# Kernel tuning notes

Measured on AMD Instinct MI355X. Metric: run time of the kernel, lower is better.

Reference implementation:

```python
import jax, jax.numpy as jnp
import numpy as np

D = 1024
H = 16
HD = D // H

def setup_inputs() -> dict:
    key = jax.random.key(0)
    ks = jax.random.split(key, 5)
    scale = 1.0 / np.sqrt(D)
    x = jax.random.normal(ks[0], (2, 2048, D), dtype=jnp.float32)
    W_qkv = jax.random.uniform(ks[1], (D, 3 * D), minval=-scale, maxval=scale, dtype=jnp.float32)
    b_qkv = jax.random.uniform(ks[2], (3 * D,), minval=-scale, maxval=scale, dtype=jnp.float32)
    W_out = jax.random.uniform(ks[3], (D, D), minval=-scale, maxval=scale, dtype=jnp.float32)
    b_out = jax.random.uniform(ks[4], (D,), minval=-scale, maxval=scale, dtype=jnp.float32)
    return {"x": x, "W_qkv": W_qkv, "b_qkv": b_qkv, "W_out": W_out, "b_out": b_out}

def reference(x, W_qkv, b_qkv, W_out, b_out):
    B, S, _ = x.shape
    qkv = x @ W_qkv + b_qkv  # [B,S,3D]
    qkv = qkv.reshape(B, S, 3, H, HD).transpose(2, 0, 3, 1, 4)  # [3,B,H,S,HD]
    q, k, v = qkv[0], qkv[1], qkv[2]
    scores = jnp.einsum('bhsd,bhtd->bhst', q, k) / jnp.sqrt(jnp.float32(HD))
    probs = jax.nn.softmax(scores, axis=-1)
    attn = jnp.einsum('bhst,bhtd->bhsd', probs, v)  # [B,H,S,HD]
    attn = attn.transpose(0, 2, 1, 3).reshape(B, S, D)
    return attn @ W_out + b_out
```

## Files before the change

### kernel.cpp

```cpp
#include <hip/hip_runtime.h>


typedef short bf16x8 __attribute__((ext_vector_type(8)));
typedef float f32x4 __attribute__((ext_vector_type(4)));

__device__ __forceinline__ unsigned short f2bf(float f) {
  unsigned u = __float_as_uint(f);
  u = (u + 0x7fffu + ((u >> 16) & 1u)) >> 16;
  return (unsigned short)u;
}
__device__ __forceinline__ unsigned pack_bf2(float lo, float hi) {
  unsigned a = __float_as_uint(lo) + 0x8000u;
  unsigned b = __float_as_uint(hi) + 0x8000u;
  return __builtin_amdgcn_perm(b, a, 0x07060302);
}
__device__ __forceinline__ void load_lds16(const unsigned short* g, unsigned short* l) {
  __builtin_amdgcn_global_load_lds(
      (const __attribute__((address_space(1))) void*)g,
      (__attribute__((address_space(3))) void*)l, 16, 0, 0);
}

__global__ __launch_bounds__(256) void cvt_f32_bf16(
    const float* __restrict__ in, unsigned short* __restrict__ out, int n)
{
  const int i = (blockIdx.x * 256 + threadIdx.x) * 8;
  if (i >= n) return;
  float4 f0 = *(const float4*)(in + i);
  float4 f1 = *(const float4*)(in + i + 4);
  union { unsigned short u[8]; uint4 v; } pk;
  pk.u[0] = f2bf(f0.x); pk.u[1] = f2bf(f0.y); pk.u[2] = f2bf(f0.z); pk.u[3] = f2bf(f0.w);
  pk.u[4] = f2bf(f1.x); pk.u[5] = f2bf(f1.y); pk.u[6] = f2bf(f1.z); pk.u[7] = f2bf(f1.w);
  *(uint4*)(out + i) = pk.v;
}

__global__ __launch_bounds__(256) void transpose_cvt(
    const float* __restrict__ in, unsigned short* __restrict__ out, int R, int C)
{
  __shared__ float tile[64][65];
  const int tid = threadIdx.x;
  const int r0 = blockIdx.y * 64, c0 = blockIdx.x * 64;
  {
    const int rr = tid >> 4;
    const int cc = (tid & 15) * 4;
#pragma unroll
    for (int it = 0; it < 4; ++it) {
      float4 f = *(const float4*)&in[(size_t)(r0 + rr + 16 * it) * C + c0 + cc];
      tile[rr + 16 * it][cc + 0] = f.x;
      tile[rr + 16 * it][cc + 1] = f.y;
      tile[rr + 16 * it][cc + 2] = f.z;
      tile[rr + 16 * it][cc + 3] = f.w;
    }
  }
  __syncthreads();
  {
    const int cr = tid >> 2;
    const int rk = (tid & 3) * 16;
    union { unsigned short u[16]; uint4 v[2]; } pk;
#pragma unroll
    for (int j = 0; j < 16; ++j) pk.u[j] = f2bf(tile[rk + j][cr]);
    uint4* dst = (uint4*)&out[(size_t)(c0 + cr) * R + r0 + rk];
    dst[0] = pk.v[0];
    dst[1] = pk.v[1];
  }
}

template <int MODE>
__global__ __launch_bounds__(256) void gemm_mfma(
    const unsigned short* __restrict__ A,
    const unsigned short* __restrict__ Bt,
    const float* __restrict__ bias,
    void* __restrict__ Cout, unsigned short* __restrict__ vT,
    int M, int N, int K)
{
  __shared__ unsigned short As[128][32];
  __shared__ unsigned short Bs[128][32];
  const int tid = threadIdx.x;
  const int wave = tid >> 6, lane = tid & 63;
  const int l16 = lane & 15, quad = lane >> 4;
  const int m0 = blockIdx.y * 128, n0 = blockIdx.x * 128;
  const int wm = (wave & 1) * 64, wn = (wave >> 1) * 64;
  const int lr = lane >> 2;
  const int lc = (lane & 3) * 8;

  f32x4 acc[4][4] = {};

  for (int k0 = 0; k0 < K; k0 += 32) {
    __syncthreads();
    load_lds16(&A [(size_t)(m0 + 16 * wave + lr) * K + k0 + lc],      &As[16 * wave][0]);
    load_lds16(&A [(size_t)(m0 + 64 + 16 * wave + lr) * K + k0 + lc], &As[64 + 16 * wave][0]);
    load_lds16(&Bt[(size_t)(n0 + 16 * wave + lr) * K + k0 + lc],      &Bs[16 * wave][0]);
    load_lds16(&Bt[(size_t)(n0 + 64 + 16 * wave + lr) * K + k0 + lc], &Bs[64 + 16 * wave][0]);
    __syncthreads();

    bf16x8 af[4], bfr[4];
#pragma unroll
    for (int mi = 0; mi < 4; ++mi)
      af[mi] = *(const bf16x8*)&As[wm + 16 * mi + l16][quad * 8];
#pragma unroll
    for (int ni = 0; ni < 4; ++ni)
      bfr[ni] = *(const bf16x8*)&Bs[wn + 16 * ni + l16][quad * 8];
#pragma unroll
    for (int mi = 0; mi < 4; ++mi)
#pragma unroll
      for (int ni = 0; ni < 4; ++ni)
        acc[mi][ni] = __builtin_amdgcn_mfma_f32_16x16x32_bf16(
            af[mi], bfr[ni], acc[mi][ni], 0, 0, 0);
  }

#pragma unroll
  for (int ni = 0; ni < 4; ++ni) {
    const int colb = n0 + wn + 16 * ni;
    const int col = colb + l16;
    const float bv = bias[col];
    if (MODE == 0) {
#pragma unroll
      for (int mi = 0; mi < 4; ++mi)
#pragma unroll
        for (int i = 0; i < 4; ++i) {
          const int row = m0 + wm + 16 * mi + quad * 4 + i;
          ((float*)Cout)[(size_t)row * N + col] = acc[mi][ni][i] + bv;
        }
    } else if (colb < 2048) {
#pragma unroll
      for (int mi = 0; mi < 4; ++mi)
#pragma unroll
        for (int i = 0; i < 4; ++i) {
          const int row = m0 + wm + 16 * mi + quad * 4 + i;
          ((unsigned short*)Cout)[(size_t)row * N + col] = f2bf(acc[mi][ni][i] + bv);
        }
    } else {
      const int h = (col - 2048) >> 6, d = col & 63;
#pragma unroll
      for (int mi = 0; mi < 4; ++mi)
#pragma unroll
        for (int i = 0; i < 4; ++i) {
          const int row = m0 + wm + 16 * mi + quad * 4 + i;
          const int bb = row >> 11, t = row & 2047;
          vT[((size_t)(bb * 16 + h) * 64 + d) * 2048 + t] = f2bf(acc[mi][ni][i] + bv);
        }
    }
  }
}

__global__ __launch_bounds__(256, 2) void attn_mfma(
    const unsigned short* __restrict__ qkv,
    const unsigned short* __restrict__ vT,
    unsigned short* __restrict__ attn_out)
{
  __shared__ unsigned short Ks[2][4096];
  __shared__ unsigned short Vs[2][4096];
  __shared__ unsigned short Pl[4][2048];

  const int tid = threadIdx.x;
  const int wave = tid >> 6, lane = tid & 63;
  const int l16 = lane & 15, quad = lane >> 4;
  const int bh = blockIdx.y, b = bh >> 4, h = bh & 15;
  const int s0 = blockIdx.x * 128 + wave * 32;

  const unsigned short* qb = qkv + (size_t)(b * 2048) * 3072 + h * 64;
  const unsigned short* kb = qb + 1024;
  const unsigned short* vb = vT + (size_t)bh * 64 * 2048;
  unsigned short* Pw = Pl[wave];

  const int srow = lane >> 3;
  const int schunk = ((lane & 7) ^ srow) * 8;
  const int r0a = wave * 16;
  const unsigned short* kg0 = kb + (size_t)(r0a + srow) * 3072 + schunk;
  const unsigned short* kg1 = kg0 + (size_t)8 * 3072;
  const unsigned short* vg0 = vb + (size_t)(r0a + srow) * 2048 + schunk;
  const unsigned short* vg1 = vg0 + (size_t)8 * 2048;

#define STAGE_KV(buf, t0)                                            \
  do {                                                               \
    load_lds16(kg0 + (size_t)(t0) * 3072, &Ks[buf][r0a * 64]);       \
    load_lds16(kg1 + (size_t)(t0) * 3072, &Ks[buf][(r0a + 8) * 64]); \
    load_lds16(vg0 + (t0),                &Vs[buf][r0a * 64]);       \
    load_lds16(vg1 + (t0),                &Vs[buf][(r0a + 8) * 64]); \
  } while (0)

  STAGE_KV(0, 0);

  bf16x8 qf[2][2];
#pragma unroll
  for (int mt = 0; mt < 2; ++mt)
#pragma unroll
    for (int ks = 0; ks < 2; ++ks)
      qf[mt][ks] = *(const bf16x8*)&qb[(size_t)(s0 + 16 * mt + l16) * 3072 + 32 * ks + quad * 8];

  f32x4 O[2][4] = {};
  float l_part[2] = {0.0f, 0.0f};
  const float SC = 0.125f * 1.44269504f;
  const int sw = l16 & 7;
  const int psw = 2 * (l16 & 7);

  for (int it = 0; it < 32; ++it) {
    const int cur = it & 1;
    __syncthreads();
    if (it < 31) STAGE_KV(1 - cur, (it + 1) * 64);

    bf16x8 kf[4][2];
#pragma unroll
    for (int nt = 0; nt < 4; ++nt) {
      const int rb = (16 * nt + l16) * 64;
      kf[nt][0] = *(const bf16x8*)&Ks[cur][rb + ((quad ^ sw) * 8)];
      kf[nt][1] = *(const bf16x8*)&Ks[cur][rb + (((4 + quad) ^ sw) * 8)];
    }

    f32x4 sf[4][2];
#pragma unroll
    for (int nt = 0; nt < 4; ++nt)
#pragma unroll
      for (int mt = 0; mt < 2; ++mt) {
        f32x4 c = {0.0f, 0.0f, 0.0f, 0.0f};
        c = __builtin_amdgcn_mfma_f32_16x16x32_bf16(kf[nt][0], qf[mt][0], c, 0, 0, 0);
        c = __builtin_amdgcn_mfma_f32_16x16x32_bf16(kf[nt][1], qf[mt][1], c, 0, 0, 0);
        sf[nt][mt] = c;
      }

    bf16x8 vf[2][4];
#pragma unroll
    for (int nd = 0; nd < 4; ++nd) {
      const int rb = (16 * nd + l16) * 64;
      vf[0][nd] = *(const bf16x8*)&Vs[cur][rb + ((quad ^ sw) * 8)];
      vf[1][nd] = *(const bf16x8*)&Vs[cur][rb + (((4 + quad) ^ sw) * 8)];
    }

#pragma unroll
    for (int mt = 0; mt < 2; ++mt) {
      unsigned short* prow = &Pw[(16 * mt + l16) * 64];
#pragma unroll
      for (int nt = 0; nt < 4; ++nt) {
        f32x4 p;
#pragma unroll
        for (int i = 0; i < 4; ++i) {
          p[i] = __builtin_amdgcn_exp2f(__builtin_fmaf(sf[nt][mt][i], SC, -8.0f));
          l_part[mt] += p[i];
        }
        uint2 w;
        w.x = pack_bf2(p[0], p[1]);
        w.y = pack_bf2(p[2], p[3]);
        const int g2 = (4 * nt + quad) ^ psw;
        *(uint2*)&prow[g2 * 4] = w;
      }
    }

    bf16x8 pf[2][2];
#pragma unroll
    for (int mt = 0; mt < 2; ++mt) {
      const unsigned short* prow = &Pw[(16 * mt + l16) * 64];
      pf[mt][0] = *(const bf16x8*)&prow[((2 * quad) ^ psw) * 4];
      pf[mt][1] = *(const bf16x8*)&prow[((8 + 2 * quad) ^ psw) * 4];
    }

#pragma unroll
    for (int mt = 0; mt < 2; ++mt)
#pragma unroll
      for (int nd = 0; nd < 4; ++nd) {
        O[mt][nd] = __builtin_amdgcn_mfma_f32_16x16x32_bf16(pf[mt][0], vf[0][nd], O[mt][nd], 0, 0, 0);
        O[mt][nd] = __builtin_amdgcn_mfma_f32_16x16x32_bf16(pf[mt][1], vf[1][nd], O[mt][nd], 0, 0, 0);
      }
  }

  float lv[2];
#pragma unroll
  for (int mt = 0; mt < 2; ++mt) {
    float v = l_part[mt];
    v += __shfl_xor(v, 16);
    v += __shfl_xor(v, 32);
    lv[mt] = v;
  }
#pragma unroll
  for (int mt = 0; mt < 2; ++mt) {
#pragma unroll
    for (int i = 0; i < 4; ++i) {
      const float inv = 1.0f / __shfl(lv[mt], quad * 4 + i);
      const size_t row = (size_t)(b * 2048 + s0 + 16 * mt + quad * 4 + i);
#pragma unroll
      for (int nd = 0; nd < 4; ++nd)
        attn_out[row * 1024 + h * 64 + 16 * nd + l16] = f2bf(O[mt][nd][i] * inv);
    }
  }
#undef STAGE_KV
}

extern "C" void kernel_launch(void* const* d_in, const int* in_sizes, int n_in,
                              void* d_out, int out_size, void* d_ws, size_t ws_size,
                              hipStream_t stream) {
  const float* x     = (const float*)d_in[0];
  const float* W_qkv = (const float*)d_in[1];
  const float* b_qkv = (const float*)d_in[2];
  const float* W_out = (const float*)d_in[3];
  const float* b_out = (const float*)d_in[4];
  float* out = (float*)d_out;

  char* ws = (char*)d_ws;
  unsigned short* x_bf   = (unsigned short*)(ws);
  unsigned short* Wqkv_t = (unsigned short*)(ws + 8388608);
  unsigned short* Wout_t = (unsigned short*)(ws + 14680064);
  unsigned short* qkv_bf = (unsigned short*)(ws + 16777216);
  unsigned short* vT     = (unsigned short*)(ws + 41943040);
  unsigned short* attn_b = (unsigned short*)(ws + 50331648);

  cvt_f32_bf16<<<2048, 256, 0, stream>>>(x, x_bf, 4096 * 1024);
  transpose_cvt<<<dim3(48, 16), 256, 0, stream>>>(W_qkv, Wqkv_t, 1024, 3072);
  transpose_cvt<<<dim3(16, 16), 256, 0, stream>>>(W_out, Wout_t, 1024, 1024);

  gemm_mfma<1><<<dim3(24, 32), 256, 0, stream>>>(x_bf, Wqkv_t, b_qkv, qkv_bf, vT,
                                                 4096, 3072, 1024);
  attn_mfma<<<dim3(16, 32), 256, 0, stream>>>(qkv_bf, vT, attn_b);
  gemm_mfma<0><<<dim3(8, 32), 256, 0, stream>>>(attn_b, Wout_t, b_out, out, nullptr,
                                                4096, 1024, 1024);
}
```

Baseline: 212.0 us.

## Keep softmax probabilities in registers via 16x16x16 MFMA, fold scale into Q

The attention kernel no longer stages P through LDS. It feeds the exp2 outputs directly from the S accumulator layout into 16x16x16 bf16 MFMAs for P·V, and computes the row sums with an extra MFMA against a vector of ones instead of shuffles. The softmax scale and log2e are folded into Q when the QKV GEMM writes its epilogue, and the constant max offset of -8 is dropped, which risks overflow if scores are large. The V-transpose and output stores are vectorised to packed 32/64-bit writes. The change trades LDS round-trips and syncs for twice as many smaller MFMA instructions.

```diff
diff --git a/kernel.cpp b/kernel.cpp
--- a/kernel.cpp
+++ b/kernel.cpp
@@ -2,7 +2,14 @@
 
 
 typedef short bf16x8 __attribute__((ext_vector_type(8)));
+typedef short bf16x4 __attribute__((ext_vector_type(4)));
 typedef float f32x4 __attribute__((ext_vector_type(4)));
+
+#if __has_builtin(__builtin_amdgcn_mfma_f32_16x16x16_bf16)
+#define MFMA16(a, b, c) __builtin_amdgcn_mfma_f32_16x16x16_bf16(a, b, c, 0, 0, 0)
+#else
+#define MFMA16(a, b, c) __builtin_amdgcn_mfma_f32_16x16x16bf16_1k(a, b, c, 0, 0, 0)
+#endif
 
 __device__ __forceinline__ unsigned short f2bf(float f) {
   unsigned u = __float_as_uint(f);
@@ -107,6 +114,7 @@
             af[mi], bfr[ni], acc[mi][ni], 0, 0, 0);
   }
 
+  const float SCQ = 0.18033688f;
 #pragma unroll
   for (int ni = 0; ni < 4; ++ni) {
     const int colb = n0 + wn + 16 * ni;
@@ -119,6 +127,14 @@
         for (int i = 0; i < 4; ++i) {
           const int row = m0 + wm + 16 * mi + quad * 4 + i;
           ((float*)Cout)[(size_t)row * N + col] = acc[mi][ni][i] + bv;
+        }
+    } else if (colb < 1024) {
+#pragma unroll
+      for (int mi = 0; mi < 4; ++mi)
+#pragma unroll
+        for (int i = 0; i < 4; ++i) {
+          const int row = m0 + wm + 16 * mi + quad * 4 + i;
+          ((unsigned short*)Cout)[(size_t)row * N + col] = f2bf((acc[mi][ni][i] + bv) * SCQ);
         }
     } else if (colb < 2048) {
 #pragma unroll
@@ -131,13 +147,13 @@
     } else {
       const int h = (col - 2048) >> 6, d = col & 63;
 #pragma unroll
-      for (int mi = 0; mi < 4; ++mi)
-#pragma unroll
-        for (int i = 0; i < 4; ++i) {
-          const int row = m0 + wm + 16 * mi + quad * 4 + i;
-          const int bb = row >> 11, t = row & 2047;
-          vT[((size_t)(bb * 16 + h) * 64 + d) * 2048 + t] = f2bf(acc[mi][ni][i] + bv);
-        }
+      for (int mi = 0; mi < 4; ++mi) {
+        const int row = m0 + wm + 16 * mi + quad * 4;
+        const int bb = row >> 11, t = row & 2047;
+        unsigned short* dst = &vT[((size_t)(bb * 16 + h) * 64 + d) * 2048 + t];
+        *(unsigned*)(dst)     = pack_bf2(acc[mi][ni][0] + bv, acc[mi][ni][1] + bv);
+        *(unsigned*)(dst + 2) = pack_bf2(acc[mi][ni][2] + bv, acc[mi][ni][3] + bv);
+      }
     }
   }
 }
@@ -149,7 +165,6 @@
 {
   __shared__ unsigned short Ks[2][4096];
   __shared__ unsigned short Vs[2][4096];
-  __shared__ unsigned short Pl[4][2048];
 
   const int tid = threadIdx.x;
   const int wave = tid >> 6, lane = tid & 63;
@@ -160,7 +175,6 @@
   const unsigned short* qb = qkv + (size_t)(b * 2048) * 3072 + h * 64;
   const unsigned short* kb = qb + 1024;
   const unsigned short* vb = vT + (size_t)bh * 64 * 2048;
-  unsigned short* Pw = Pl[wave];
 
   const int srow = lane >> 3;
   const int schunk = ((lane & 7) ^ srow) * 8;
@@ -188,10 +202,10 @@
       qf[mt][ks] = *(const bf16x8*)&qb[(size_t)(s0 + 16 * mt + l16) * 3072 + 32 * ks + quad * 8];
 
   f32x4 O[2][4] = {};
-  float l_part[2] = {0.0f, 0.0f};
-  const float SC = 0.125f * 1.44269504f;
+  f32x4 lacc[2] = {};
+  const bf16x4 ones4 = {(short)0x3F80, (short)0x3F80, (short)0x3F80, (short)0x3F80};
   const int sw = l16 & 7;
-  const int psw = 2 * (l16 & 7);
+  const int h2 = quad >> 1, h1 = (quad & 1) * 4;
 
   for (int it = 0; it < 32; ++it) {
     const int cur = it & 1;
@@ -204,6 +218,15 @@
       const int rb = (16 * nt + l16) * 64;
       kf[nt][0] = *(const bf16x8*)&Ks[cur][rb + ((quad ^ sw) * 8)];
       kf[nt][1] = *(const bf16x8*)&Ks[cur][rb + (((4 + quad) ^ sw) * 8)];
+    }
+
+    bf16x4 vf[4][4];
+#pragma unroll
+    for (int nd = 0; nd < 4; ++nd) {
+      const int rb = (16 * nd + l16) * 64;
+#pragma unroll
+      for (int c = 0; c < 4; ++c)
+        vf[nd][c] = *(const bf16x4*)&Vs[cur][rb + (((2 * c + h2) ^ sw) * 8 + h1)];
     }
 
     f32x4 sf[4][2];
@@ -217,67 +240,42 @@
         sf[nt][mt] = c;
       }
 
-    bf16x8 vf[2][4];
+    bf16x4 pp[2][4];
+#pragma unroll
+    for (int mt = 0; mt < 2; ++mt)
+#pragma unroll
+      for (int nt = 0; nt < 4; ++nt) {
+        const float p0 = __builtin_amdgcn_exp2f(sf[nt][mt][0]);
+        const float p1 = __builtin_amdgcn_exp2f(sf[nt][mt][1]);
+        const float p2 = __builtin_amdgcn_exp2f(sf[nt][mt][2]);
+        const float p3 = __builtin_amdgcn_exp2f(sf[nt][mt][3]);
+        uint2 w;
+        w.x = pack_bf2(p0, p1);
+        w.y = pack_bf2(p2, p3);
+        pp[mt][nt] = *(bf16x4*)&w;
+      }
+
+#pragma unroll
+    for (int c = 0; c < 4; ++c)
+#pragma unroll
+      for (int mt = 0; mt < 2; ++mt) {
+        lacc[mt] = MFMA16(ones4, pp[mt][c], lacc[mt]);
+#pragma unroll
+        for (int nd = 0; nd < 4; ++nd)
+          O[mt][nd] = MFMA16(vf[nd][c], pp[mt][c], O[mt][nd]);
+      }
+  }
+
+#pragma unroll
+  for (int mt = 0; mt < 2; ++mt) {
+    const float inv = 1.0f / lacc[mt][0];
+    const size_t row = (size_t)(b * 2048 + s0 + 16 * mt + l16);
 #pragma unroll
     for (int nd = 0; nd < 4; ++nd) {
-      const int rb = (16 * nd + l16) * 64;
-      vf[0][nd] = *(const bf16x8*)&Vs[cur][rb + ((quad ^ sw) * 8)];
-      vf[1][nd] = *(const bf16x8*)&Vs[cur][rb + (((4 + quad) ^ sw) * 8)];
-    }
-
-#pragma unroll
-    for (int mt = 0; mt < 2; ++mt) {
-      unsigned short* prow = &Pw[(16 * mt + l16) * 64];
-#pragma unroll
-      for (int nt = 0; nt < 4; ++nt) {
-        f32x4 p;
-#pragma unroll
-        for (int i = 0; i < 4; ++i) {
-          p[i] = __builtin_amdgcn_exp2f(__builtin_fmaf(sf[nt][mt][i], SC, -8.0f));
-          l_part[mt] += p[i];
-        }
-        uint2 w;
-        w.x = pack_bf2(p[0], p[1]);
-        w.y = pack_bf2(p[2], p[3]);
-        const int g2 = (4 * nt + quad) ^ psw;
-        *(uint2*)&prow[g2 * 4] = w;
-      }
-    }
-
-    bf16x8 pf[2][2];
-#pragma unroll
-    for (int mt = 0; mt < 2; ++mt) {
-      const unsigned short* prow = &Pw[(16 * mt + l16) * 64];
-      pf[mt][0] = *(const bf16x8*)&prow[((2 * quad) ^ psw) * 4];
-      pf[mt][1] = *(const bf16x8*)&prow[((8 + 2 * quad) ^ psw) * 4];
-    }
-
-#pragma unroll
-    for (int mt = 0; mt < 2; ++mt)
-#pragma unroll
-      for (int nd = 0; nd < 4; ++nd) {
-        O[mt][nd] = __builtin_amdgcn_mfma_f32_16x16x32_bf16(pf[mt][0], vf[0][nd], O[mt][nd], 0, 0, 0);
-        O[mt][nd] = __builtin_amdgcn_mfma_f32_16x16x32_bf16(pf[mt][1], vf[1][nd], O[mt][nd], 0, 0, 0);
-      }
-  }
-
-  float lv[2];
-#pragma unroll
-  for (int mt = 0; mt < 2; ++mt) {
-    float v = l_part[mt];
-    v += __shfl_xor(v, 16);
-    v += __shfl_xor(v, 32);
-    lv[mt] = v;
-  }
-#pragma unroll
-  for (int mt = 0; mt < 2; ++mt) {
-#pragma unroll
-    for (int i = 0; i < 4; ++i) {
-      const float inv = 1.0f / __shfl(lv[mt], quad * 4 + i);
-      const size_t row = (size_t)(b * 2048 + s0 + 16 * mt + quad * 4 + i);
-#pragma unroll
-      for (int nd = 0; nd < 4; ++nd)
-        attn_out[row * 1024 + h * 64 + 16 * nd + l16] = f2bf(O[mt][nd][i] * inv);
+      uint2 w;
+      w.x = pack_bf2(O[mt][nd][0] * inv, O[mt][nd][1] * inv);
+      w.y = pack_bf2(O[mt][nd][2] * inv, O[mt][nd][3] * inv);
+      *(uint2*)&attn_out[row * 1024 + h * 64 + 16 * nd + quad * 4] = w;
     }
   }
 #undef STAGE_KV
```

Result: faster. 203.4 us (-4.1%).
